# Kernel tuning notes

Measured on AMD Instinct MI355X. Metric: run time of the kernel, lower is better.

## Reference

```python
import jax, jax.numpy as jnp
import numpy as np

N, E, B, O = 100000, 1600000, 256, 32
D, H, OD = 128, 128, 32  # node_features, hidden_dim, order_encoding_dim
L = 3  # num_layers


def setup_inputs() -> dict:
    key = jax.random.key(0)
    ks = jax.random.split(key, 32)
    g = lambda k, s, fan: jax.random.normal(k, s, jnp.float32) * (1.0 / np.sqrt(fan))
    inp = {
        'x': jax.random.normal(ks[0], (N, D), jnp.float32),
        'edge_index': jax.random.randint(ks[1], (2, E), 0, N),
        'orders': jax.random.normal(ks[2], (B, O, OD), jnp.float32),
        'batch': jnp.sort(jax.random.randint(ks[3], (N,), 0, B)),
        # GIN layers (input_dim == hidden_dim so all 3 layers stack): MLP = Lin(H,H)->ReLU->Lin(H,H), then BatchNorm1d
        'gW1': g(ks[4], (L, H, H), H), 'gb1': jnp.zeros((L, H)),
        'gW2': g(ks[5], (L, H, H), H), 'gb2': jnp.zeros((L, H)),
        'gamma': jnp.ones((L, H)), 'beta': jnp.zeros((L, H)),
        # order encoder: Lin(OD,H)->ReLU->Lin(H,H)
        'oW1': g(ks[6], (OD, H), OD), 'ob1': jnp.zeros((H,)),
        'oW2': g(ks[7], (H, H), H), 'ob2': jnp.zeros((H,)),
        # score head: Lin(4H,H)->ReLU->Lin(H,H//2)->ReLU->Lin(H//2,1)
        'sW1': g(ks[8], (4 * H, H), 4 * H), 'sb1': jnp.zeros((H,)),
        'sW2': g(ks[9], (H, H // 2), H), 'sb2': jnp.zeros((H // 2,)),
        'sW3': g(ks[10], (H // 2, 1), H // 2), 'sb3': jnp.zeros((1,)),
    }
    return inp


def reference(x, edge_index, orders, batch, gW1, gb1, gW2, gb2, gamma, beta,
              oW1, ob1, oW2, ob2, sW1, sb1, sW2, sb2, sW3, sb3):
    n = x.shape[0]
    src, dst = edge_index[0], edge_index[1]
    h = x
    nl = gW1.shape[0]
    for i in range(nl):  # fixed small layer count
        agg = jax.ops.segment_sum(h[src], dst, num_segments=n)  # sum aggregation
        z = agg + h  # (1 + eps) * x with eps = 0 (GINConv default)
        z = jnp.maximum(z @ gW1[i] + gb1[i], 0) @ gW2[i] + gb2[i]
        mu = z.mean(0)
        var = z.var(0)  # biased var, as torch BN uses for normalization
        z = (z - mu) * jax.lax.rsqrt(var + 1e-5) * gamma[i] + beta[i]
        h = jnp.maximum(z, 0) if i < nl - 1 else z  # dropout inactive (eval)
    b = orders.shape[0]
    cnt = jax.ops.segment_sum(jnp.ones((n,), h.dtype), batch, num_segments=b)
    ssum = jax.ops.segment_sum(h, batch, num_segments=b)
    smean = ssum / jnp.maximum(cnt, 1)[:, None]
    smax = jax.ops.segment_max(h, batch, num_segments=b)
    smax = jnp.where(jnp.isfinite(smax), smax, 0)
    graph = jnp.concatenate([smean, smax, ssum], axis=-1)  # [B, 3H]
    # batched over num_orders (equivalent to the python per-order loop)
    oe = jnp.maximum(orders @ oW1 + ob1, 0) @ oW2 + ob2  # [B, O, H]
    comb = jnp.concatenate(
        [jnp.broadcast_to(graph[:, None, :], (b, orders.shape[1], graph.shape[-1])), oe], axis=-1)
    s = jnp.maximum(comb @ sW1 + sb1, 0)
    s = jnp.maximum(s @ sW2 + sb2, 0)
    s = (s @ sW3 + sb3)[..., 0]  # [B, O]
    return s
```

## Files before the change

kernel.cpp:

```cpp
#include <hip/hip_runtime.h>

static constexpr int NN = 100000;
static constexpr int NE = 1600000;
static constexpr int NB = 256;
static constexpr int NO = 32;
static constexpr int HD = 128;
static constexpr long NH = (long)NN * HD;

static constexpr int BSHIFT = 9;
static constexpr int BSIZE = 1 << BSHIFT;
static constexpr int NBUCK = 256;
static constexpr int CHUNK = 16384;
static constexpr int NCHUNK = (NE + CHUNK - 1) / CHUNK;
static constexpr int POOL_ROWS = 64;
static constexpr int POOL_GRID = (NN + POOL_ROWS - 1) / POOL_ROWS;
static constexpr int NSUB = 64;

typedef _Float16 f16x8 __attribute__((ext_vector_type(8)));
typedef _Float16 f16x4 __attribute__((ext_vector_type(4)));
typedef _Float16 f16x2 __attribute__((ext_vector_type(2)));
typedef float f32x4 __attribute__((ext_vector_type(4)));

__device__ __forceinline__ unsigned int encf(float f) {
  unsigned int u = __float_as_uint(f);
  return (u & 0x80000000u) ? ~u : (u | 0x80000000u);
}
__device__ __forceinline__ float decf(unsigned int e) {
  return (e & 0x80000000u) ? __uint_as_float(e & 0x7fffffffu) : __uint_as_float(~e);
}

__global__ void bucket_count(const int* __restrict__ ei, int* __restrict__ bucketTotal) {
  __shared__ int cnt[NBUCK];
  const int t = threadIdx.x;
  cnt[t] = 0;
  __syncthreads();
  long start = (long)blockIdx.x * CHUNK;
  long end = min((long)NE, start + CHUNK);
  for (long e = start + t; e < end; e += 256)
    atomicAdd(&cnt[ei[NE + e] >> BSHIFT], 1);
  __syncthreads();
  if (cnt[t]) atomicAdd(&bucketTotal[t], cnt[t]);
}

__global__ void bucket_scan(const int* __restrict__ bucketTotal, int* __restrict__ bucketBase,
                            int* __restrict__ cursor) {
  __shared__ int part[NBUCK];
  const int t = threadIdx.x;
  int v = bucketTotal[t];
  part[t] = v;
  __syncthreads();
  for (int off = 1; off < NBUCK; off <<= 1) {
    int u = (t >= off) ? part[t - off] : 0;
    __syncthreads();
    part[t] += u;
    __syncthreads();
  }
  int base = part[t] - v;
  bucketBase[t] = base;
  cursor[t] = base;
  if (t == NBUCK - 1) bucketBase[NBUCK] = part[t];
}

__global__ void bucket_scatter(const int* __restrict__ ei, int* __restrict__ cursor,
                               unsigned int* __restrict__ binned) {
  __shared__ int cnt[NBUCK];
  __shared__ int runbase[NBUCK];
  const int t = threadIdx.x;
  cnt[t] = 0;
  __syncthreads();
  long start = (long)blockIdx.x * CHUNK;
  long end = min((long)NE, start + CHUNK);
  for (long e = start + t; e < end; e += 256)
    atomicAdd(&cnt[ei[NE + e] >> BSHIFT], 1);
  __syncthreads();
  int c = cnt[t];
  runbase[t] = c ? atomicAdd(&cursor[t], c) : 0;
  cnt[t] = 0;
  __syncthreads();
  for (long e = start + t; e < end; e += 256) {
    int d = ei[NE + e], s = ei[e];
    int b = d >> BSHIFT;
    int pos = runbase[b] + atomicAdd(&cnt[b], 1);
    binned[pos] = ((unsigned int)s << BSHIFT) | (unsigned int)(d & (BSIZE - 1));
  }
}

__global__ void bucket_csr(const unsigned int* __restrict__ binned,
                           const int* __restrict__ bucketBase,
                           int* __restrict__ rowptr, int* __restrict__ col) {
  __shared__ int cnt[BSIZE];
  __shared__ int excl[BSIZE];
  __shared__ int cur[BSIZE];
  __shared__ int part[256];
  const int b = blockIdx.x;
  const int t = threadIdx.x;
  const int lo = bucketBase[b], hi = bucketBase[b + 1];
  cnt[t] = 0; cnt[t + 256] = 0;
  __syncthreads();
  for (int i = lo + t; i < hi; i += 256)
    atomicAdd(&cnt[binned[i] & (BSIZE - 1)], 1);
  __syncthreads();
  int a0 = cnt[2 * t], a1 = cnt[2 * t + 1];
  int s = a0 + a1;
  part[t] = s;
  __syncthreads();
  for (int off = 1; off < 256; off <<= 1) {
    int u = (t >= off) ? part[t - off] : 0;
    __syncthreads();
    part[t] += u;
    __syncthreads();
  }
  int ebase = part[t] - s;
  excl[2 * t] = ebase;
  excl[2 * t + 1] = ebase + a0;
  __syncthreads();
  const int node0 = b * BSIZE;
  for (int i = t; i < BSIZE; i += 256) {
    int node = node0 + i;
    if (node < NN) rowptr[node] = lo + excl[i] + cnt[i];
    cur[i] = lo + excl[i];
  }
  __syncthreads();
  for (int i = lo + t; i < hi; i += 256) {
    unsigned int v = binned[i];
    int pos = atomicAdd(&cur[v & (BSIZE - 1)], 1);
    col[pos] = (int)(v >> BSHIFT);
  }
}

__global__ void f32to16_kernel(const float* __restrict__ in, _Float16* __restrict__ out) {
  long i = (long)(blockIdx.x * 256 + threadIdx.x) * 8;
  if (i >= NH) return;
  float4 a = *reinterpret_cast<const float4*>(in + i);
  float4 b = *reinterpret_cast<const float4*>(in + i + 4);
  f16x8 v;
  v[0] = (_Float16)a.x; v[1] = (_Float16)a.y; v[2] = (_Float16)a.z; v[3] = (_Float16)a.w;
  v[4] = (_Float16)b.x; v[5] = (_Float16)b.y; v[6] = (_Float16)b.z; v[7] = (_Float16)b.w;
  *reinterpret_cast<f16x8*>(out + i) = v;
}

__global__ void pack_w_kernel(const float* __restrict__ gW1, const float* __restrict__ gW2,
                              _Float16* __restrict__ Wp) {
  int tid = blockIdx.x * blockDim.x + threadIdx.x;
  if (tid >= 12288) return;
  int lane = tid & 63;
  int s = (tid >> 6) & 3;
  int t = (tid >> 8) & 7;
  int which = (tid >> 11) & 1;
  int layer = tid >> 12;
  const float* W = (which ? gW2 : gW1) + (long)layer * 128 * 128;
  _Float16* dst = Wp + (long)tid * 8;
  int kbase = s * 32 + ((lane >> 4) << 3);
  int n = t * 16 + (lane & 15);
#pragma unroll
  for (int j = 0; j < 8; ++j) dst[j] = (_Float16)W[(kbase + j) * 128 + n];
}

__global__ void pack_head_kernel(const float* __restrict__ oW1, const float* __restrict__ oW2,
                                 const float* __restrict__ sW1, const float* __restrict__ sW2,
                                 _Float16* __restrict__ dst) {
  int tid = blockIdx.x * blockDim.x + threadIdx.x;
  if (tid >= 5632) return;
  const float* W; int K, N, rowOff;
  int base = tid;
  if (tid < 512)       { W = oW1; K = 32;  N = 128; rowOff = 0;   }
  else if (tid < 2560) { W = oW2; K = 128; N = 128; rowOff = 0;   base = tid - 512; }
  else if (tid < 4608) { W = sW1; K = 128; N = 128; rowOff = 384; base = tid - 2560; }
  else                 { W = sW2; K = 128; N = 64;  rowOff = 0;   base = tid - 4608; }
  int lane = base & 63;
  int fs = base >> 6;
  int NS = K >> 5;
  int s = fs % NS;
  int tt = fs / NS;
  int k = s * 32 + ((lane >> 4) << 3);
  int n = tt * 16 + (lane & 15);
  _Float16* d = dst + (long)tid * 8;
#pragma unroll
  for (int j = 0; j < 8; ++j) d[j] = (_Float16)W[(long)(rowOff + k + j) * N + n];
}

template <bool BN, bool RELU>
__global__ void gather_kernel(const _Float16* __restrict__ hin, const int* __restrict__ rowptr,
                              const int* __restrict__ col, const float* __restrict__ accum,
                              const float* __restrict__ gamma, const float* __restrict__ beta,
                              _Float16* __restrict__ z) {
  const int node = (blockIdx.x * blockDim.x + threadIdx.x) >> 6;
  if (node >= NN) return;
  const int c2 = (threadIdx.x & 63) * 2;
  float scx = 1.f, scy = 1.f, shx = 0.f, shy = 0.f;
  if (BN) {
    const float n = (float)NN;
    float mu0 = accum[c2] / n, mu1 = accum[c2 + 1] / n;
    float v0 = accum[128 + c2] / n - mu0 * mu0;
    float v1 = accum[128 + c2 + 1] / n - mu1 * mu1;
    scx = rsqrtf(v0 + 1e-5f) * gamma[c2];
    scy = rsqrtf(v1 + 1e-5f) * gamma[c2 + 1];
    shx = beta[c2] - mu0 * scx;
    shy = beta[c2 + 1] - mu1 * scy;
  }
  auto ldh = [&](int n) -> float2 {
    f16x2 h = *reinterpret_cast<const f16x2*>(hin + (long)n * HD + c2);
    float2 v = make_float2((float)h[0], (float)h[1]);
    if (BN) {
      v.x = fmaf(v.x, scx, shx);
      v.y = fmaf(v.y, scy, shy);
      if (RELU) { v.x = fmaxf(v.x, 0.f); v.y = fmaxf(v.y, 0.f); }
    }
    return v;
  };
  const int lo = (node == 0) ? 0 : rowptr[node - 1];
  const int hi = rowptr[node];
  float2 acc = ldh(node);
  int j = lo;
  for (; j + 4 <= hi; j += 4) {
    int s0 = col[j], s1 = col[j + 1], s2 = col[j + 2], s3 = col[j + 3];
    float2 v0 = ldh(s0), v1 = ldh(s1), v2 = ldh(s2), v3 = ldh(s3);
    acc.x += (v0.x + v1.x) + (v2.x + v3.x);
    acc.y += (v0.y + v1.y) + (v2.y + v3.y);
  }
  if (j < hi) {
    int last = hi - 1;
    int s0 = col[j];
    int s1 = col[min(j + 1, last)];
    int s2 = col[min(j + 2, last)];
    int s3 = col[min(j + 3, last)];
    float m1 = (j + 1 < hi) ? 1.f : 0.f;
    float m2 = (j + 2 < hi) ? 1.f : 0.f;
    float m3 = (j + 3 < hi) ? 1.f : 0.f;
    float2 v0 = ldh(s0), v1 = ldh(s1), v2 = ldh(s2), v3 = ldh(s3);
    acc.x += v0.x + m1 * v1.x + m2 * v2.x + m3 * v3.x;
    acc.y += v0.y + m1 * v1.y + m2 * v2.y + m3 * v3.y;
  }
  f16x2 o;
  o[0] = (_Float16)acc.x;
  o[1] = (_Float16)acc.y;
  *reinterpret_cast<f16x2*>(z + (long)node * HD + c2) = o;
}

__global__ void __launch_bounds__(256)
fused_layer(const _Float16* __restrict__ Z, const _Float16* __restrict__ Wp,
            const float* __restrict__ b1, const float* __restrict__ b2,
            _Float16* __restrict__ Z2, float* __restrict__ accum2) {
  __shared__ _Float16 Abuf[64 * 136];
  __shared__ float red[256];
  const int t = threadIdx.x;
  const int row0 = blockIdx.x * 64;
  const int lane = t & 63;
  const int w = t >> 6;
  const int l15 = lane & 15;
  const int kgrp = lane >> 4;

  for (int idx = t; idx < 64 * 16; idx += 256) {
    int r = idx >> 4;
    int c8 = (idx & 15) * 8;
    int row = row0 + r;
    f16x8 v = {};
    if (row < NN) v = *reinterpret_cast<const f16x8*>(Z + (long)row * HD + c8);
    *reinterpret_cast<f16x8*>(&Abuf[r * 136 + c8]) = v;
  }
  red[t] = 0.f;
  __syncthreads();

  f32x4 acc[8];
  {
    f16x8 af[4];
#pragma unroll
    for (int s = 0; s < 4; ++s)
      af[s] = *reinterpret_cast<const f16x8*>(&Abuf[(w * 16 + l15) * 136 + s * 32 + kgrp * 8]);
    const _Float16* W1p = Wp;
#pragma unroll
    for (int tt = 0; tt < 8; ++tt) {
      float bb = b1[tt * 16 + l15];
      acc[tt] = (f32x4){bb, bb, bb, bb};
#pragma unroll
      for (int s = 0; s < 4; ++s) {
        f16x8 bf = *reinterpret_cast<const f16x8*>(W1p + ((tt * 4 + s) * 64 + lane) * 8);
        acc[tt] = __builtin_amdgcn_mfma_f32_16x16x32_f16(af[s], bf, acc[tt], 0, 0, 0);
      }
    }
  }
#pragma unroll
  for (int tt = 0; tt < 8; ++tt) {
#pragma unroll
    for (int j = 0; j < 4; ++j) {
      float v = fmaxf(acc[tt][j], 0.f);
      Abuf[(w * 16 + kgrp * 4 + j) * 136 + tt * 16 + l15] = (_Float16)v;
    }
  }
  {
    f16x8 af[4];
#pragma unroll
    for (int s = 0; s < 4; ++s)
      af[s] = *reinterpret_cast<const f16x8*>(&Abuf[(w * 16 + l15) * 136 + s * 32 + kgrp * 8]);
    const _Float16* W2p = Wp + 16384;
#pragma unroll
    for (int tt = 0; tt < 8; ++tt) {
      float bb = b2[tt * 16 + l15];
      acc[tt] = (f32x4){bb, bb, bb, bb};
#pragma unroll
      for (int s = 0; s < 4; ++s) {
        f16x8 bf = *reinterpret_cast<const f16x8*>(W2p + ((tt * 4 + s) * 64 + lane) * 8);
        acc[tt] = __builtin_amdgcn_mfma_f32_16x16x32_f16(af[s], bf, acc[tt], 0, 0, 0);
      }
    }
  }
#pragma unroll
  for (int tt = 0; tt < 8; ++tt) {
    int c = tt * 16 + l15;
    float s = 0.f, q = 0.f;
#pragma unroll
    for (int j = 0; j < 4; ++j) {
      int r = row0 + w * 16 + kgrp * 4 + j;
      if (r < NN) {
        float v = acc[tt][j];
        Z2[(long)r * HD + c] = (_Float16)v;
        s += v; q += v * v;
      }
    }
    atomicAdd(&red[c], s);
    atomicAdd(&red[128 + c], q);
  }
  __syncthreads();
  atomicAdd(&accum2[(blockIdx.x & (NSUB - 1)) * 256 + t], red[t]);
}

__global__ void bn_reduce(const float* __restrict__ accum2, float* __restrict__ accum) {
  const int c = threadIdx.x;
  float s = 0.f;
  for (int i = 0; i < NSUB; ++i) s += accum2[i * 256 + c];
  accum[c] = s;
}

__global__ void pool_init(float* __restrict__ ssum, unsigned int* __restrict__ smaxU) {
  int i = blockIdx.x * 256 + threadIdx.x;
  ssum[i] = 0.f;
  smaxU[i] = 0x007FFFFFu;
}

__global__ void pool_partial(const _Float16* __restrict__ z2, const float* __restrict__ accum,
                             const float* __restrict__ gamma, const float* __restrict__ beta,
                             const int* __restrict__ batch,
                             float* __restrict__ ssum, unsigned int* __restrict__ smaxU) {
  const int c = threadIdx.x;
  const int row0 = blockIdx.x * POOL_ROWS;
  const int rowEnd = min(row0 + POOL_ROWS, NN);
  const float n = (float)NN;
  float mu = accum[c] / n;
  float var = accum[128 + c] / n - mu * mu;
  const float sc = rsqrtf(var + 1e-5f) * gamma[c];
  const float sh = beta[c] - mu * sc;

  int curb = batch[row0];
  float s = 0.f, m = -INFINITY;
  for (int row = row0; row < rowEnd; ++row) {
    int b = batch[row];
    if (b != curb) {
      atomicAdd(&ssum[curb * HD + c], s);
      atomicMax(&smaxU[curb * HD + c], encf(m));
      s = 0.f; m = -INFINITY; curb = b;
    }
    float v = fmaf((float)z2[(long)row * HD + c], sc, sh);
    s += v;
    m = fmaxf(m, v);
  }
  atomicAdd(&ssum[curb * HD + c], s);
  atomicMax(&smaxU[curb * HD + c], encf(m));
}

__global__ void pool_final(const int* __restrict__ batch, float* __restrict__ ssum,
                           unsigned int* __restrict__ smaxU, float* __restrict__ smean,
                           float* __restrict__ smax) {
  const int b = blockIdx.x;
  const int c = threadIdx.x;
  int lo = 0, hi = NN;
  while (lo < hi) { int mid = (lo + hi) >> 1; if (batch[mid] < b) lo = mid + 1; else hi = mid; }
  const int start = lo;
  hi = NN;
  while (lo < hi) { int mid = (lo + hi) >> 1; if (batch[mid] < b + 1) lo = mid + 1; else hi = mid; }
  const int cnt = lo - start;
  float s = ssum[b * HD + c];
  smean[b * HD + c] = s / fmaxf((float)cnt, 1.f);
  smax[b * HD + c] = (cnt > 0) ? decf(smaxU[b * HD + c]) : 0.f;
}

__global__ void gpart_kernel(const float* __restrict__ smean, const float* __restrict__ smax,
                             const float* __restrict__ ssum, const float* __restrict__ sW1,
                             const float* __restrict__ sb1, float* __restrict__ gpart) {
  const int b = blockIdx.x;
  const int j = threadIdx.x;
  float acc = sb1[j];
  for (int k = 0; k < 128; ++k) acc = fmaf(smean[b * HD + k], sW1[k * 128 + j], acc);
  for (int k = 0; k < 128; ++k) acc = fmaf(smax[b * HD + k], sW1[(128 + k) * 128 + j], acc);
  for (int k = 0; k < 128; ++k) acc = fmaf(ssum[b * HD + k], sW1[(256 + k) * 128 + j], acc);
  gpart[b * HD + j] = acc;
}

__global__ void __launch_bounds__(128)
head_mfma(const float* __restrict__ orders, const _Float16* __restrict__ Wh,
          const float* __restrict__ ob1, const float* __restrict__ ob2,
          const float* __restrict__ gpart, const float* __restrict__ sb2,
          const float* __restrict__ sW3, const float* __restrict__ sb3,
          float* __restrict__ out) {
  __shared__ _Float16 B1[32 * 136];
  __shared__ _Float16 B2[32 * 136];
  const int t = threadIdx.x;
  const int g = blockIdx.x;
  const int row0 = g * 32;
  const int lane = t & 63;
  const int w = t >> 6;
  const int l15 = lane & 15;
  const int kgrp = lane >> 4;
  const _Float16* oW1p  = Wh;
  const _Float16* oW2p  = Wh + 4096;
  const _Float16* sW1bp = Wh + 20480;
  const _Float16* sW2p  = Wh + 36864;

  for (int idx = t; idx < 32 * 8; idx += 128) {
    int r = idx >> 3;
    int c4 = (idx & 7) * 4;
    float4 v = *reinterpret_cast<const float4*>(orders + (long)(row0 + r) * 32 + c4);
    f16x4 h;
    h[0] = (_Float16)v.x; h[1] = (_Float16)v.y; h[2] = (_Float16)v.z; h[3] = (_Float16)v.w;
    *reinterpret_cast<f16x4*>(&B1[r * 136 + c4]) = h;
  }
  __syncthreads();

  f32x4 acc[8];
  {
    f16x8 a0 = *reinterpret_cast<const f16x8*>(&B1[(w * 16 + l15) * 136 + kgrp * 8]);
#pragma unroll
    for (int tt = 0; tt < 8; ++tt) {
      float bb = ob1[tt * 16 + l15];
      acc[tt] = (f32x4){bb, bb, bb, bb};
      f16x8 bf = *reinterpret_cast<const f16x8*>(oW1p + (tt * 64 + lane) * 8);
      acc[tt] = __builtin_amdgcn_mfma_f32_16x16x32_f16(a0, bf, acc[tt], 0, 0, 0);
    }
#pragma unroll
    for (int tt = 0; tt < 8; ++tt)
#pragma unroll
      for (int j = 0; j < 4; ++j)
        B2[(w * 16 + kgrp * 4 + j) * 136 + tt * 16 + l15] = (_Float16)fmaxf(acc[tt][j], 0.f);
  }
  {
    f16x8 af[4];
#pragma unroll
    for (int s = 0; s < 4; ++s)
      af[s] = *reinterpret_cast<const f16x8*>(&B2[(w * 16 + l15) * 136 + s * 32 + kgrp * 8]);
#pragma unroll
    for (int tt = 0; tt < 8; ++tt) {
      float bb = ob2[tt * 16 + l15];
      acc[tt] = (f32x4){bb, bb, bb, bb};
#pragma unroll
      for (int s = 0; s < 4; ++s) {
        f16x8 bf = *reinterpret_cast<const f16x8*>(oW2p + ((tt * 4 + s) * 64 + lane) * 8);
        acc[tt] = __builtin_amdgcn_mfma_f32_16x16x32_f16(af[s], bf, acc[tt], 0, 0, 0);
      }
    }
#pragma unroll
    for (int tt = 0; tt < 8; ++tt)
#pragma unroll
      for (int j = 0; j < 4; ++j)
        B1[(w * 16 + kgrp * 4 + j) * 136 + tt * 16 + l15] = (_Float16)acc[tt][j];
  }
  {
    f16x8 af[4];
#pragma unroll
    for (int s = 0; s < 4; ++s)
      af[s] = *reinterpret_cast<const f16x8*>(&B1[(w * 16 + l15) * 136 + s * 32 + kgrp * 8]);
#pragma unroll
    for (int tt = 0; tt < 8; ++tt) {
      acc[tt] = (f32x4){0.f, 0.f, 0.f, 0.f};
#pragma unroll
      for (int s = 0; s < 4; ++s) {
        f16x8 bf = *reinterpret_cast<const f16x8*>(sW1bp + ((tt * 4 + s) * 64 + lane) * 8);
        acc[tt] = __builtin_amdgcn_mfma_f32_16x16x32_f16(af[s], bf, acc[tt], 0, 0, 0);
      }
    }
#pragma unroll
    for (int tt = 0; tt < 8; ++tt) {
      int c = tt * 16 + l15;
      float gp = gpart[g * HD + c];
#pragma unroll
      for (int j = 0; j < 4; ++j)
        B2[(w * 16 + kgrp * 4 + j) * 136 + c] = (_Float16)fmaxf(acc[tt][j] + gp, 0.f);
    }
  }
  {
    f16x8 af[4];
#pragma unroll
    for (int s = 0; s < 4; ++s)
      af[s] = *reinterpret_cast<const f16x8*>(&B2[(w * 16 + l15) * 136 + s * 32 + kgrp * 8]);
#pragma unroll
    for (int tt = 0; tt < 4; ++tt) {
      float bb = sb2[tt * 16 + l15];
      acc[tt] = (f32x4){bb, bb, bb, bb};
#pragma unroll
      for (int s = 0; s < 4; ++s) {
        f16x8 bf = *reinterpret_cast<const f16x8*>(sW2p + ((tt * 4 + s) * 64 + lane) * 8);
        acc[tt] = __builtin_amdgcn_mfma_f32_16x16x32_f16(af[s], bf, acc[tt], 0, 0, 0);
      }
    }
    float rsum[4] = {0.f, 0.f, 0.f, 0.f};
#pragma unroll
    for (int tt = 0; tt < 4; ++tt) {
      float wv = sW3[tt * 16 + l15];
#pragma unroll
      for (int j = 0; j < 4; ++j)
        rsum[j] = fmaf(fmaxf(acc[tt][j], 0.f), wv, rsum[j]);
    }
#pragma unroll
    for (int j = 0; j < 4; ++j) {
      rsum[j] += __shfl_xor(rsum[j], 1);
      rsum[j] += __shfl_xor(rsum[j], 2);
      rsum[j] += __shfl_xor(rsum[j], 4);
      rsum[j] += __shfl_xor(rsum[j], 8);
    }
    if (l15 == 0) {
      float b3 = sb3[0];
#pragma unroll
      for (int j = 0; j < 4; ++j)
        out[row0 + w * 16 + kgrp * 4 + j] = rsum[j] + b3;
    }
  }
}

extern "C" void kernel_launch(void* const* d_in, const int* in_sizes, int n_in,
                              void* d_out, int out_size, void* d_ws, size_t ws_size,
                              hipStream_t stream) {
  const float* x      = (const float*)d_in[0];
  const int*   ei     = (const int*)d_in[1];
  const float* orders = (const float*)d_in[2];
  const int*   batch  = (const int*)d_in[3];
  const float* gW1    = (const float*)d_in[4];
  const float* gb1    = (const float*)d_in[5];
  const float* gW2    = (const float*)d_in[6];
  const float* gb2    = (const float*)d_in[7];
  const float* gamma  = (const float*)d_in[8];
  const float* beta   = (const float*)d_in[9];
  const float* oW1    = (const float*)d_in[10];
  const float* ob1    = (const float*)d_in[11];
  const float* oW2    = (const float*)d_in[12];
  const float* ob2    = (const float*)d_in[13];
  const float* sW1    = (const float*)d_in[14];
  const float* sb1    = (const float*)d_in[15];
  const float* sW2    = (const float*)d_in[16];
  const float* sb2    = (const float*)d_in[17];
  const float* sW3    = (const float*)d_in[18];
  const float* sb3    = (const float*)d_in[19];
  float* out = (float*)d_out;

  char* ws = (char*)d_ws;
  _Float16* xh    = (_Float16*)ws;
  _Float16* bufAh = xh + NH;
  _Float16* bufCh = bufAh + NH;
  float* accum  = (float*)(bufCh + NH);
  float* accum2 = accum + 256;
  float* ssum   = accum2 + NSUB * 256;
  float* smean  = ssum + NB * HD;
  float* smax   = smean + NB * HD;
  unsigned int* smaxU = (unsigned int*)(smax + NB * HD);
  float* gpart = (float*)(smaxU + NB * HD);
  int* rowptr = (int*)(gpart + NB * HD);
  int* col    = rowptr + NN;
  unsigned int* binned = (unsigned int*)(col + NE);
  int* bucketTotal = (int*)(binned + NE);
  int* bucketBase  = bucketTotal + NBUCK;
  int* cursor      = bucketBase + NBUCK + 1;
  _Float16* Wp  = (_Float16*)(cursor + NBUCK);
  _Float16* Wh  = Wp + 3 * 32768;

  hipMemsetAsync(bucketTotal, 0, NBUCK * sizeof(int), stream);
  bucket_count<<<NCHUNK, 256, 0, stream>>>(ei, bucketTotal);
  bucket_scan<<<1, NBUCK, 0, stream>>>(bucketTotal, bucketBase, cursor);
  bucket_scatter<<<NCHUNK, 256, 0, stream>>>(ei, cursor, binned);
  bucket_csr<<<NBUCK, 256, 0, stream>>>(binned, bucketBase, rowptr, col);

  pack_w_kernel<<<48, 256, 0, stream>>>(gW1, gW2, Wp);
  pack_head_kernel<<<22, 256, 0, stream>>>(oW1, oW2, sW1, sW2, Wh);
  f32to16_kernel<<<(int)(NH / 8 + 255) / 256, 256, 0, stream>>>(x, xh);

  const int GATHER_GRID = NN / 4;
  const int LAYER_GRID = (NN + 63) / 64;
  for (int l = 0; l < 3; ++l) {
    if (l == 0)
      gather_kernel<false, false><<<GATHER_GRID, 256, 0, stream>>>(
          xh, rowptr, col, accum, gamma, beta, bufAh);
    else
      gather_kernel<true, true><<<GATHER_GRID, 256, 0, stream>>>(
          bufCh, rowptr, col, accum, gamma + (l - 1) * 128, beta + (l - 1) * 128, bufAh);
    hipMemsetAsync(accum2, 0, NSUB * 256 * sizeof(float), stream);
    fused_layer<<<LAYER_GRID, 256, 0, stream>>>(
        bufAh, Wp + (long)l * 32768, gb1 + l * 128, gb2 + l * 128, bufCh, accum2);
    bn_reduce<<<1, 256, 0, stream>>>(accum2, accum);
  }

  pool_init<<<128, 256, 0, stream>>>(ssum, smaxU);
  pool_partial<<<POOL_GRID, 128, 0, stream>>>(bufCh, accum, gamma + 2 * 128, beta + 2 * 128,
                                              batch, ssum, smaxU);
  pool_final<<<NB, 128, 0, stream>>>(batch, ssum, smaxU, smean, smax);

  gpart_kernel<<<NB, 128, 0, stream>>>(smean, smax, ssum, sW1, sb1, gpart);
  head_mfma<<<NB, 128, 0, stream>>>(orders, Wh, ob1, ob2, gpart, sb2, sW3, sb3, out);
}
```

Measured before the change: 552.0 us.

## Use fixed-capacity buckets for CSR build and apply BatchNorm in a separate pass

```diff
diff --git a/kernel.cpp b/kernel.cpp
--- a/kernel.cpp
+++ b/kernel.cpp
@@ -10,11 +10,13 @@
 static constexpr int BSHIFT = 9;
 static constexpr int BSIZE = 1 << BSHIFT;
 static constexpr int NBUCK = 256;
+static constexpr int BCAP = 10240;
 static constexpr int CHUNK = 16384;
 static constexpr int NCHUNK = (NE + CHUNK - 1) / CHUNK;
 static constexpr int POOL_ROWS = 64;
 static constexpr int POOL_GRID = (NN + POOL_ROWS - 1) / POOL_ROWS;
 static constexpr int NSUB = 64;
+static constexpr int GATHER_GRID = NN / 4;
 
 typedef _Float16 f16x8 __attribute__((ext_vector_type(8)));
 typedef _Float16 f16x4 __attribute__((ext_vector_type(4)));
@@ -27,38 +29,6 @@
 }
 __device__ __forceinline__ float decf(unsigned int e) {
   return (e & 0x80000000u) ? __uint_as_float(e & 0x7fffffffu) : __uint_as_float(~e);
-}
-
-__global__ void bucket_count(const int* __restrict__ ei, int* __restrict__ bucketTotal) {
-  __shared__ int cnt[NBUCK];
-  const int t = threadIdx.x;
-  cnt[t] = 0;
-  __syncthreads();
-  long start = (long)blockIdx.x * CHUNK;
-  long end = min((long)NE, start + CHUNK);
-  for (long e = start + t; e < end; e += 256)
-    atomicAdd(&cnt[ei[NE + e] >> BSHIFT], 1);
-  __syncthreads();
-  if (cnt[t]) atomicAdd(&bucketTotal[t], cnt[t]);
-}
-
-__global__ void bucket_scan(const int* __restrict__ bucketTotal, int* __restrict__ bucketBase,
-                            int* __restrict__ cursor) {
-  __shared__ int part[NBUCK];
-  const int t = threadIdx.x;
-  int v = bucketTotal[t];
-  part[t] = v;
-  __syncthreads();
-  for (int off = 1; off < NBUCK; off <<= 1) {
-    int u = (t >= off) ? part[t - off] : 0;
-    __syncthreads();
-    part[t] += u;
-    __syncthreads();
-  }
-  int base = part[t] - v;
-  bucketBase[t] = base;
-  cursor[t] = base;
-  if (t == NBUCK - 1) bucketBase[NBUCK] = part[t];
 }
 
 __global__ void bucket_scatter(const int* __restrict__ ei, int* __restrict__ cursor,
@@ -80,21 +50,23 @@
   for (long e = start + t; e < end; e += 256) {
     int d = ei[NE + e], s = ei[e];
     int b = d >> BSHIFT;
-    int pos = runbase[b] + atomicAdd(&cnt[b], 1);
+    int pos = b * BCAP + runbase[b] + atomicAdd(&cnt[b], 1);
     binned[pos] = ((unsigned int)s << BSHIFT) | (unsigned int)(d & (BSIZE - 1));
   }
 }
 
 __global__ void bucket_csr(const unsigned int* __restrict__ binned,
-                           const int* __restrict__ bucketBase,
-                           int* __restrict__ rowptr, int* __restrict__ col) {
+                           const int* __restrict__ cursor,
+                           int* __restrict__ rowStart, int* __restrict__ rowEnd,
+                           int* __restrict__ col) {
   __shared__ int cnt[BSIZE];
   __shared__ int excl[BSIZE];
   __shared__ int cur[BSIZE];
   __shared__ int part[256];
   const int b = blockIdx.x;
   const int t = threadIdx.x;
-  const int lo = bucketBase[b], hi = bucketBase[b + 1];
+  const int lo = b * BCAP;
+  const int hi = lo + cursor[b];
   cnt[t] = 0; cnt[t + 256] = 0;
   __syncthreads();
   for (int i = lo + t; i < hi; i += 256)
@@ -117,7 +89,10 @@
   const int node0 = b * BSIZE;
   for (int i = t; i < BSIZE; i += 256) {
     int node = node0 + i;
-    if (node < NN) rowptr[node] = lo + excl[i] + cnt[i];
+    if (node < NN) {
+      rowStart[node] = lo + excl[i];
+      rowEnd[node]   = lo + excl[i] + cnt[i];
+    }
     cur[i] = lo + excl[i];
   }
   __syncthreads();
@@ -179,37 +154,18 @@
   for (int j = 0; j < 8; ++j) d[j] = (_Float16)W[(long)(rowOff + k + j) * N + n];
 }
 
-template <bool BN, bool RELU>
-__global__ void gather_kernel(const _Float16* __restrict__ hin, const int* __restrict__ rowptr,
-                              const int* __restrict__ col, const float* __restrict__ accum,
-                              const float* __restrict__ gamma, const float* __restrict__ beta,
+__global__ void gather_kernel(const _Float16* __restrict__ hin, const int* __restrict__ rowStart,
+                              const int* __restrict__ rowEnd, const int* __restrict__ col,
                               _Float16* __restrict__ z) {
   const int node = (blockIdx.x * blockDim.x + threadIdx.x) >> 6;
   if (node >= NN) return;
   const int c2 = (threadIdx.x & 63) * 2;
-  float scx = 1.f, scy = 1.f, shx = 0.f, shy = 0.f;
-  if (BN) {
-    const float n = (float)NN;
-    float mu0 = accum[c2] / n, mu1 = accum[c2 + 1] / n;
-    float v0 = accum[128 + c2] / n - mu0 * mu0;
-    float v1 = accum[128 + c2 + 1] / n - mu1 * mu1;
-    scx = rsqrtf(v0 + 1e-5f) * gamma[c2];
-    scy = rsqrtf(v1 + 1e-5f) * gamma[c2 + 1];
-    shx = beta[c2] - mu0 * scx;
-    shy = beta[c2 + 1] - mu1 * scy;
-  }
   auto ldh = [&](int n) -> float2 {
     f16x2 h = *reinterpret_cast<const f16x2*>(hin + (long)n * HD + c2);
-    float2 v = make_float2((float)h[0], (float)h[1]);
-    if (BN) {
-      v.x = fmaf(v.x, scx, shx);
-      v.y = fmaf(v.y, scy, shy);
-      if (RELU) { v.x = fmaxf(v.x, 0.f); v.y = fmaxf(v.y, 0.f); }
-    }
-    return v;
+    return make_float2((float)h[0], (float)h[1]);
   };
-  const int lo = (node == 0) ? 0 : rowptr[node - 1];
-  const int hi = rowptr[node];
+  const int lo = rowStart[node];
+  const int hi = rowEnd[node];
   float2 acc = ldh(node);
   int j = lo;
   for (; j + 4 <= hi; j += 4) {
@@ -324,11 +280,44 @@
   atomicAdd(&accum2[(blockIdx.x & (NSUB - 1)) * 256 + t], red[t]);
 }
 
-__global__ void bn_reduce(const float* __restrict__ accum2, float* __restrict__ accum) {
+__global__ void bn_reduce(const float* __restrict__ accum2, const float* __restrict__ gamma,
+                          const float* __restrict__ beta, float* __restrict__ scsh) {
   const int c = threadIdx.x;
   float s = 0.f;
   for (int i = 0; i < NSUB; ++i) s += accum2[i * 256 + c];
-  accum[c] = s;
+  __shared__ float red[256];
+  red[c] = s;
+  __syncthreads();
+  if (c < 128) {
+    const float n = (float)NN;
+    float mu = red[c] / n;
+    float var = red[128 + c] / n - mu * mu;
+    float sc = rsqrtf(var + 1e-5f) * gamma[c];
+    scsh[c] = sc;
+    scsh[128 + c] = beta[c] - mu * sc;
+  }
+}
+
+__global__ void bn_apply(const _Float16* __restrict__ z2, const float* __restrict__ scsh,
+                         _Float16* __restrict__ hn) {
+  long idx = (long)blockIdx.x * 256 + threadIdx.x;
+  if (idx >= (long)NN * 16) return;
+  int c8 = ((int)idx & 15) * 8;
+  float4 sc0 = *reinterpret_cast<const float4*>(scsh + c8);
+  float4 sc1 = *reinterpret_cast<const float4*>(scsh + c8 + 4);
+  float4 sh0 = *reinterpret_cast<const float4*>(scsh + 128 + c8);
+  float4 sh1 = *reinterpret_cast<const float4*>(scsh + 128 + c8 + 4);
+  f16x8 v = *reinterpret_cast<const f16x8*>(z2 + idx * 8);
+  f16x8 o;
+  o[0] = (_Float16)fmaxf(fmaf((float)v[0], sc0.x, sh0.x), 0.f);
+  o[1] = (_Float16)fmaxf(fmaf((float)v[1], sc0.y, sh0.y), 0.f);
+  o[2] = (_Float16)fmaxf(fmaf((float)v[2], sc0.z, sh0.z), 0.f);
+  o[3] = (_Float16)fmaxf(fmaf((float)v[3], sc0.w, sh0.w), 0.f);
+  o[4] = (_Float16)fmaxf(fmaf((float)v[4], sc1.x, sh1.x), 0.f);
+  o[5] = (_Float16)fmaxf(fmaf((float)v[5], sc1.y, sh1.y), 0.f);
+  o[6] = (_Float16)fmaxf(fmaf((float)v[6], sc1.z, sh1.z), 0.f);
+  o[7] = (_Float16)fmaxf(fmaf((float)v[7], sc1.w, sh1.w), 0.f);
+  *reinterpret_cast<f16x8*>(hn + idx * 8) = o;
 }
 
 __global__ void pool_init(float* __restrict__ ssum, unsigned int* __restrict__ smaxU) {
@@ -337,18 +326,14 @@
   smaxU[i] = 0x007FFFFFu;
 }
 
-__global__ void pool_partial(const _Float16* __restrict__ z2, const float* __restrict__ accum,
-                             const float* __restrict__ gamma, const float* __restrict__ beta,
+__global__ void pool_partial(const _Float16* __restrict__ z2, const float* __restrict__ scsh,
                              const int* __restrict__ batch,
                              float* __restrict__ ssum, unsigned int* __restrict__ smaxU) {
   const int c = threadIdx.x;
   const int row0 = blockIdx.x * POOL_ROWS;
   const int rowEnd = min(row0 + POOL_ROWS, NN);
-  const float n = (float)NN;
-  float mu = accum[c] / n;
-  float var = accum[128 + c] / n - mu * mu;
-  const float sc = rsqrtf(var + 1e-5f) * gamma[c];
-  const float sh = beta[c] - mu * sc;
+  const float sc = scsh[c];
+  const float sh = scsh[128 + c];
 
   int curb = batch[row0];
   float s = 0.f, m = -INFINITY;
@@ -553,50 +538,42 @@
   _Float16* xh    = (_Float16*)ws;
   _Float16* bufAh = xh + NH;
   _Float16* bufCh = bufAh + NH;
-  float* accum  = (float*)(bufCh + NH);
-  float* accum2 = accum + 256;
-  float* ssum   = accum2 + NSUB * 256;
+  float* accum2 = (float*)(bufCh + NH);
+  float* scsh   = accum2 + NSUB * 256;
+  float* ssum   = scsh + 256;
   float* smean  = ssum + NB * HD;
   float* smax   = smean + NB * HD;
   unsigned int* smaxU = (unsigned int*)(smax + NB * HD);
   float* gpart = (float*)(smaxU + NB * HD);
-  int* rowptr = (int*)(gpart + NB * HD);
-  int* col    = rowptr + NN;
-  unsigned int* binned = (unsigned int*)(col + NE);
-  int* bucketTotal = (int*)(binned + NE);
-  int* bucketBase  = bucketTotal + NBUCK;
-  int* cursor      = bucketBase + NBUCK + 1;
+  int* rowStart = (int*)(gpart + NB * HD);
+  int* rowEnd   = rowStart + NN;
+  int* col      = rowEnd + NN;
+  unsigned int* binned = (unsigned int*)(col + NBUCK * BCAP);
+  int* cursor = (int*)(binned + NBUCK * BCAP);
   _Float16* Wp  = (_Float16*)(cursor + NBUCK);
   _Float16* Wh  = Wp + 3 * 32768;
 
-  hipMemsetAsync(bucketTotal, 0, NBUCK * sizeof(int), stream);
-  bucket_count<<<NCHUNK, 256, 0, stream>>>(ei, bucketTotal);
-  bucket_scan<<<1, NBUCK, 0, stream>>>(bucketTotal, bucketBase, cursor);
+  hipMemsetAsync(cursor, 0, NBUCK * sizeof(int), stream);
   bucket_scatter<<<NCHUNK, 256, 0, stream>>>(ei, cursor, binned);
-  bucket_csr<<<NBUCK, 256, 0, stream>>>(binned, bucketBase, rowptr, col);
+  bucket_csr<<<NBUCK, 256, 0, stream>>>(binned, cursor, rowStart, rowEnd, col);
 
   pack_w_kernel<<<48, 256, 0, stream>>>(gW1, gW2, Wp);
   pack_head_kernel<<<22, 256, 0, stream>>>(oW1, oW2, sW1, sW2, Wh);
   f32to16_kernel<<<(int)(NH / 8 + 255) / 256, 256, 0, stream>>>(x, xh);
 
-  const int GATHER_GRID = NN / 4;
   const int LAYER_GRID = (NN + 63) / 64;
+  const int BA_GRID = (int)((NN * 16 + 255) / 256);
   for (int l = 0; l < 3; ++l) {
-    if (l == 0)
-      gather_kernel<false, false><<<GATHER_GRID, 256, 0, stream>>>(
-          xh, rowptr, col, accum, gamma, beta, bufAh);
-    else
-      gather_kernel<true, true><<<GATHER_GRID, 256, 0, stream>>>(
-          bufCh, rowptr, col, accum, gamma + (l - 1) * 128, beta + (l - 1) * 128, bufAh);
+    gather_kernel<<<GATHER_GRID, 256, 0, stream>>>(xh, rowStart, rowEnd, col, bufAh);
     hipMemsetAsync(accum2, 0, NSUB * 256 * sizeof(float), stream);
     fused_layer<<<LAYER_GRID, 256, 0, stream>>>(
         bufAh, Wp + (long)l * 32768, gb1 + l * 128, gb2 + l * 128, bufCh, accum2);
-    bn_reduce<<<1, 256, 0, stream>>>(accum2, accum);
+    bn_reduce<<<1, 256, 0, stream>>>(accum2, gamma + l * 128, beta + l * 128, scsh);
+    if (l < 2) bn_apply<<<BA_GRID, 256, 0, stream>>>(bufCh, scsh, xh);
   }
 
   pool_init<<<128, 256, 0, stream>>>(ssum, smaxU);
-  pool_partial<<<POOL_GRID, 128, 0, stream>>>(bufCh, accum, gamma + 2 * 128, beta + 2 * 128,
-                                              batch, ssum, smaxU);
+  pool_partial<<<POOL_GRID, 128, 0, stream>>>(bufCh, scsh, batch, ssum, smaxU);
   pool_final<<<NB, 128, 0, stream>>>(batch, ssum, smaxU, smean, smax);
 
   gpart_kernel<<<NB, 128, 0, stream>>>(smean, smax, ssum, sW1, sb1, gpart);
```

After: 550.3 us. Within noise of the previous version (-0.3%).
